# Optimization experiments

Hardware: AMD Instinct MI355X
Metric: run time of the kernel (lower is better)

The kernel has to match this reference:

```python
import jax, jax.numpy as jnp
import numpy as np

B, D, L = 16, 64, 2048
NUM_TOKENS = 8192


def setup_inputs() -> dict:
    key = jax.random.key(0)
    k1, k2 = jax.random.split(key)
    z_e = jax.random.normal(k1, (B, D, L), dtype=jnp.float32)
    codebook = jax.random.normal(k2, (NUM_TOKENS, D), dtype=jnp.float32)
    return {"z_e": z_e, "codebook": codebook}


def reference(z_e, codebook):
    # z_e: [B, D, L] -> per-position vectors [B, L, D]
    x = jnp.transpose(z_e, (0, 2, 1))          # [B, L, D]
    xf = x.reshape(-1, x.shape[-1])            # [N, D], N = B*L
    x2 = jnp.sum(xf * xf, axis=-1, keepdims=True)            # [N, 1]
    c2 = jnp.sum(codebook * codebook, axis=-1)               # [K]
    d2 = x2 - 2.0 * (xf @ codebook.T) + c2[None, :]          # [N, K]
    idx = jnp.argmin(d2, axis=-1)                            # [N]
    zq = codebook[idx]                                        # [N, D] gather
    zq = zq.reshape(x.shape)                                  # [B, L, D]
    # straight-through with codebook stop-gradient (code_sg=True)
    zq_st = x + jax.lax.stop_gradient(zq - x)                 # [B, L, D]
    v_q = jnp.transpose(zq_st, (0, 2, 1))                     # [B, D, L]
    indices = idx.reshape(z_e.shape[0], -1)                   # [B, L]
    return v_q, indices
```

## Files before the change

kernel.cpp:

```cpp
#include <hip/hip_runtime.h>
#include <hip/hip_bf16.h>
#include <cstdint>

#define BB 16
#define DD 64
#define LL 2048
#define NQ (BB*LL)
#define KK 8192
#define VQ_SIZE (BB*DD*LL)
#define CHUNK 256
#define NCH (KK/CHUNK)
#define QSL 256
#define QPS (NQ/QSL)
#define MARGIN 0.75f

typedef __attribute__((ext_vector_type(8))) short short8;
typedef __attribute__((ext_vector_type(4))) float f32x4;
typedef unsigned long long u64;


static __device__ inline short f2bf(float f) {
    __hip_bfloat16 h = __float2bfloat16(f);
    return __builtin_bit_cast(short, h);
}

#define FMIN_DPP(v, ctrl)                                                     \
    do {                                                                      \
        int _vi = __float_as_int(v);                                          \
        int _sh = __builtin_amdgcn_update_dpp(_vi, _vi, (ctrl), 0xf, 0xf, false); \
        (v) = fminf((v), __int_as_float(_sh));                                \
    } while (0)

#define FMAX_DPP(v, ctrl)                                                     \
    do {                                                                      \
        int _vi = __float_as_int(v);                                          \
        int _sh = __builtin_amdgcn_update_dpp(_vi, _vi, (ctrl), 0xf, 0xf, false); \
        (v) = fmaxf((v), __int_as_float(_sh));                                \
    } while (0)

__global__ __launch_bounds__(256) void prep_x(const float* __restrict__ ze,
                                              short* __restrict__ xb) {
    __shared__ float t[64][65];
    const int b = blockIdx.x;
    const int l0 = blockIdx.y * 64;
    const int tid = threadIdx.x;
    #pragma unroll
    for (int it = 0; it < 4; ++it) {
        int id = it * 256 + tid;
        int d = id >> 4;
        int lw = (id & 15) * 4;
        const float4 v = *(const float4*)(ze + ((size_t)b * DD + d) * LL + l0 + lw);
        t[d][lw + 0] = v.x; t[d][lw + 1] = v.y; t[d][lw + 2] = v.z; t[d][lw + 3] = v.w;
    }
    __syncthreads();
    #pragma unroll
    for (int it = 0; it < 2; ++it) {
        int id = it * 256 + tid;
        int lr = id >> 3;
        int u = id & 7;
        short8 o;
        #pragma unroll
        for (int e = 0; e < 8; ++e) o[e] = f2bf(t[u * 8 + e][lr]);
        *(short8*)(xb + (size_t)(b * LL + l0 + lr) * DD + u * 8) = o;
    }
}

__global__ __launch_bounds__(256) void prep_xf(const float* __restrict__ ze,
                                               float* __restrict__ xf) {
    __shared__ float t[64][65];
    const int b = blockIdx.x;
    const int l0 = blockIdx.y * 64;
    const int tid = threadIdx.x;
    #pragma unroll
    for (int it = 0; it < 4; ++it) {
        int id = it * 256 + tid;
        int d = id >> 4;
        int lw = (id & 15) * 4;
        const float4 v = *(const float4*)(ze + ((size_t)b * DD + d) * LL + l0 + lw);
        t[d][lw + 0] = v.x; t[d][lw + 1] = v.y; t[d][lw + 2] = v.z; t[d][lw + 3] = v.w;
    }
    __syncthreads();
    #pragma unroll
    for (int it = 0; it < 4; ++it) {
        int id = it * 256 + tid;
        int row = id >> 4;
        int u = id & 15;
        float4 o = make_float4(t[4 * u + 0][row], t[4 * u + 1][row],
                               t[4 * u + 2][row], t[4 * u + 3][row]);
        *(float4*)(xf + (size_t)(b * LL + l0 + row) * DD + u * 4) = o;
    }
}

__global__ __launch_bounds__(256) void prep_nh2(const float* __restrict__ cbf,
                                                float* __restrict__ nh2) {
    int k = blockIdx.x * 256 + threadIdx.x;
    const float4* c4 = (const float4*)(cbf + (size_t)k * DD);
    float s = 0.f;
    #pragma unroll
    for (int i = 0; i < DD / 4; ++i) {
        float4 v = c4[i];
        s += v.x * v.x + v.y * v.y + v.z * v.z + v.w * v.w;
    }
    nh2[k] = -0.5f * s;
}

__global__ __launch_bounds__(256) void vq_screen(const float* __restrict__ cbf,
                                                 const float* __restrict__ nh2,
                                                 const short* __restrict__ xb,
                                                 float* __restrict__ cmaxT) {
    __shared__ short cbt[CHUNK * 64];
    __shared__ float sh2[CHUNK];
    const int tid = threadIdx.x;
    const int lane = tid & 63;
    const int wid = tid >> 6;
    const int kbase = blockIdx.y * CHUNK;
    const int qbase = blockIdx.x * 512 + wid * 128;
    const int r16 = lane & 15, g = lane >> 4;

    #pragma unroll
    for (int it = 0; it < 8; ++it) {
        int id = it * 256 + tid;
        int row = id >> 3;
        int u = id & 7;
        const float4 lo = *(const float4*)(cbf + (size_t)(kbase + row) * 64 + u * 8);
        const float4 hi = *(const float4*)(cbf + (size_t)(kbase + row) * 64 + u * 8 + 4);
        short8 o;
        o[0] = f2bf(lo.x); o[1] = f2bf(lo.y); o[2] = f2bf(lo.z); o[3] = f2bf(lo.w);
        o[4] = f2bf(hi.x); o[5] = f2bf(hi.y); o[6] = f2bf(hi.z); o[7] = f2bf(hi.w);
        *(short8*)(&cbt[row * 64 + ((u ^ (row & 7)) * 8)]) = o;
    }
    sh2[tid] = nh2[kbase + tid];
    __syncthreads();

    short8 a[8][2];
    #pragma unroll
    for (int t = 0; t < 8; ++t)
        #pragma unroll
        for (int ks = 0; ks < 2; ++ks)
            a[t][ks] = *(const short8*)(xb + (size_t)(qbase + t * 16 + r16) * 64 + ks * 32 + g * 8);

    float rm[8][4];
    #pragma unroll
    for (int t = 0; t < 8; ++t)
        #pragma unroll
        for (int j = 0; j < 4; ++j) rm[t][j] = -3.4e38f;

    for (int cs = 0; cs < CHUNK / 16; ++cs) {
        const int rowb = cs * 16 + r16;
        const float nh = sh2[rowb];
        const f32x4 ci = {nh, nh, nh, nh};
        const short8 b0 = *(const short8*)(&cbt[rowb * 64 + ((g ^ (rowb & 7)) * 8)]);
        const short8 b1 = *(const short8*)(&cbt[rowb * 64 + (((g + 4) ^ (rowb & 7)) * 8)]);
        #pragma unroll
        for (int t = 0; t < 8; ++t) {
            f32x4 acc = __builtin_amdgcn_mfma_f32_16x16x32_bf16(a[t][0], b0, ci, 0, 0, 0);
            acc = __builtin_amdgcn_mfma_f32_16x16x32_bf16(a[t][1], b1, acc, 0, 0, 0);
            rm[t][0] = fmaxf(rm[t][0], acc[0]);
            rm[t][1] = fmaxf(rm[t][1], acc[1]);
            rm[t][2] = fmaxf(rm[t][2], acc[2]);
            rm[t][3] = fmaxf(rm[t][3], acc[3]);
        }
    }

    #pragma unroll
    for (int t = 0; t < 8; ++t)
        #pragma unroll
        for (int j = 0; j < 4; ++j) {
            FMAX_DPP(rm[t][j], 0x111);
            FMAX_DPP(rm[t][j], 0x112);
            FMAX_DPP(rm[t][j], 0x114);
            FMAX_DPP(rm[t][j], 0x118);
        }

    if (r16 == 15) {
        #pragma unroll
        for (int t = 0; t < 8; ++t)
            #pragma unroll
            for (int j = 0; j < 4; ++j)
                cmaxT[(size_t)blockIdx.y * NQ + (qbase + t * 16 + g * 4 + j)] = rm[t][j];
    }
}

__global__ __launch_bounds__(256) void vq_cand(const float* __restrict__ cmaxT,
                                               u64* __restrict__ qmask,
                                               u64* __restrict__ keys) {
    const int tid = threadIdx.x;
    const int lane = tid & 63;
    const int q = blockIdx.x * 256 + tid;
    const int qword = q >> 6;
    float v[NCH];
    float m = -3.4e38f;
    #pragma unroll
    for (int j = 0; j < NCH; ++j) {
        v[j] = cmaxT[(size_t)j * NQ + q];
        m = fmaxf(m, v[j]);
    }
    keys[q] = ~0ULL;
    const float thr = m - MARGIN;
    #pragma unroll
    for (int j = 0; j < NCH; ++j) {
        u64 mm = __ballot(v[j] >= thr);
        if (lane == 0) qmask[(size_t)j * (NQ / 64) + qword] = mm;
    }
}

__global__ __launch_bounds__(256, 2) void vq_exact(const float* __restrict__ xf,
                                                   const float* __restrict__ cbf,
                                                   const float* __restrict__ nh2,
                                                   const u64* __restrict__ qmask,
                                                   u64* __restrict__ keys) {
    const int ch = blockIdx.x;
    const int slice = blockIdx.y;
    const int lane = threadIdx.x & 63;
    const int wid = threadIdx.x >> 6;
    const int kb = ch * CHUNK + wid * 64;
    const int k = kb + lane;

    const u64* wm = qmask + (size_t)ch * (NQ / 64) + slice * (QPS / 64);
    u64 words[QPS / 64];
    u64 any = 0;
    #pragma unroll
    for (int w = 0; w < QPS / 64; ++w) {
        u64 x = wm[w];
        uint32_t lo = __builtin_amdgcn_readfirstlane((uint32_t)x);
        uint32_t hi = __builtin_amdgcn_readfirstlane((uint32_t)(x >> 32));
        words[w] = ((u64)hi << 32) | lo;
        any |= words[w];
    }
    if (!any) return;

    f32x4 cdv[16];
    const f32x4* cb4 = (const f32x4*)(cbf + (size_t)k * DD);
    #pragma unroll
    for (int i = 0; i < 16; ++i) cdv[i] = cb4[i];
    const float nh2k = nh2[k];

    #pragma unroll 1
    for (int w = 0; w < QPS / 64; ++w) {
        u64 sw = words[w];
        while (sw) {
            const int bit = __ffsll((long long)sw) - 1;
            sw &= sw - 1;
            const int q = slice * QPS + w * 64 + bit;
            const f32x4* xr4 = (const f32x4*)(xf + (size_t)q * DD);
            f32x4 xv[16];
            #pragma unroll
            for (int i = 0; i < 16; ++i) xv[i] = xr4[i];

            float a0 = 0.f, a1 = 0.f, a2 = 0.f, a3 = 0.f;
            #pragma unroll
            for (int i = 0; i < 16; ++i) {
                a0 = fmaf(xv[i].x, cdv[i].x, a0);
                a1 = fmaf(xv[i].y, cdv[i].y, a1);
                a2 = fmaf(xv[i].z, cdv[i].z, a2);
                a3 = fmaf(xv[i].w, cdv[i].w, a3);
            }
            float val = -(((a0 + a1) + (a2 + a3)) + nh2k);

            float mn = val;
            FMIN_DPP(mn, 0x111);
            FMIN_DPP(mn, 0x112);
            FMIN_DPP(mn, 0x114);
            FMIN_DPP(mn, 0x118);
            FMIN_DPP(mn, 0x142);
            FMIN_DPP(mn, 0x143);
            const float mnall = __uint_as_float(
                __builtin_amdgcn_readlane(__float_as_uint(mn), 63));

            u64 mk = __ballot(val == mnall);
            int srcl = __ffsll((long long)mk) - 1;
            uint32_t uu = __float_as_uint(mnall);
            uint32_t ub = ((int)uu < 0) ? ~uu : (uu | 0x80000000u);
            u64 key = ((u64)ub << 32) | (unsigned)(kb + srcl);
            if (lane == 0) atomicMin(&keys[q], key);
        }
    }
}

__global__ __launch_bounds__(256) void vq_gather(const float* __restrict__ cb,
                                                 const u64* __restrict__ keys,
                                                 float* __restrict__ vq,
                                                 float* __restrict__ oidx) {
    int t = blockIdx.x * 256 + threadIdx.x;
    int l = t & (LL - 1);
    int bd = t >> 11;
    int d = bd & 63;
    int b = bd >> 6;
    int idx = (int)(unsigned)(keys[b * LL + l] & 0x1FFFu);
    vq[t] = cb[idx * DD + d];
    if (d == 0) oidx[b * LL + l] = (float)idx;
}

extern "C" void kernel_launch(void* const* d_in, const int* in_sizes, int n_in,
                              void* d_out, int out_size, void* d_ws, size_t ws_size,
                              hipStream_t stream) {
    const float* ze = (const float*)d_in[0];
    const float* cb = (const float*)d_in[1];
    float* out = (float*)d_out;

    short* xb = (short*)d_out;
    float* cmaxT = (float*)((char*)d_out + (size_t)NQ * DD * 2);
    float* xf = (float*)d_out;
    u64* qmask = (u64*)(out + VQ_SIZE);
    float* nh2 = (float*)d_ws;
    u64* keys = (u64*)((char*)d_ws + (size_t)KK * 4);
    float* oidx = out + VQ_SIZE;

    dim3 gx(BB, LL / 64);
    prep_x<<<gx, 256, 0, stream>>>(ze, xb);
    prep_nh2<<<KK / 256, 256, 0, stream>>>(cb, nh2);

    dim3 gs(NQ / 512, NCH);
    vq_screen<<<gs, 256, 0, stream>>>(cb, nh2, xb, cmaxT);

    vq_cand<<<NQ / 256, 256, 0, stream>>>(cmaxT, qmask, keys);

    prep_xf<<<gx, 256, 0, stream>>>(ze, xf);

    dim3 ge(NCH, QSL);
    vq_exact<<<ge, 256, 0, stream>>>(xf, cb, nh2, qmask, keys);

    vq_gather<<<VQ_SIZE / 256, 256, 0, stream>>>(cb, keys, out, oidx);
}
```

Baseline: 153.8 us.

## Screen codebook at 128-entry granularity with fp16 maxima and per-query masks

Result: slower. 158.7 us (+3.1%).

```diff
diff --git a/kernel.cpp b/kernel.cpp
--- a/kernel.cpp
+++ b/kernel.cpp
@@ -1,5 +1,6 @@
 #include <hip/hip_runtime.h>
 #include <hip/hip_bf16.h>
+#include <hip/hip_fp16.h>
 #include <cstdint>
 
 #define BB 16
@@ -10,9 +11,10 @@
 #define VQ_SIZE (BB*DD*LL)
 #define CHUNK 256
 #define NCH (KK/CHUNK)
+#define NG 64
 #define QSL 256
 #define QPS (NQ/QSL)
-#define MARGIN 0.75f
+#define MARGIN 0.80f
 
 typedef __attribute__((ext_vector_type(8))) short short8;
 typedef __attribute__((ext_vector_type(4))) float f32x4;
@@ -107,14 +109,14 @@
 __global__ __launch_bounds__(256) void vq_screen(const float* __restrict__ cbf,
                                                  const float* __restrict__ nh2,
                                                  const short* __restrict__ xb,
-                                                 float* __restrict__ cmaxT) {
+                                                 __half* __restrict__ cmaxG) {
     __shared__ short cbt[CHUNK * 64];
     __shared__ float sh2[CHUNK];
     const int tid = threadIdx.x;
     const int lane = tid & 63;
     const int wid = tid >> 6;
     const int kbase = blockIdx.y * CHUNK;
-    const int qbase = blockIdx.x * 512 + wid * 128;
+    const int qbase = blockIdx.x * 256 + wid * 64;
     const int r16 = lane & 15, g = lane >> 4;
 
     #pragma unroll
@@ -132,19 +134,22 @@
     sh2[tid] = nh2[kbase + tid];
     __syncthreads();
 
-    short8 a[8][2];
-    #pragma unroll
-    for (int t = 0; t < 8; ++t)
+    short8 a[4][2];
+    #pragma unroll
+    for (int t = 0; t < 4; ++t)
         #pragma unroll
         for (int ks = 0; ks < 2; ++ks)
             a[t][ks] = *(const short8*)(xb + (size_t)(qbase + t * 16 + r16) * 64 + ks * 32 + g * 8);
 
-    float rm[8][4];
-    #pragma unroll
-    for (int t = 0; t < 8; ++t)
-        #pragma unroll
-        for (int j = 0; j < 4; ++j) rm[t][j] = -3.4e38f;
-
+    float rm[2][4][4];
+    #pragma unroll
+    for (int h = 0; h < 2; ++h)
+        #pragma unroll
+        for (int t = 0; t < 4; ++t)
+            #pragma unroll
+            for (int j = 0; j < 4; ++j) rm[h][t][j] = -3.4e38f;
+
+    #pragma unroll
     for (int cs = 0; cs < CHUNK / 16; ++cs) {
         const int rowb = cs * 16 + r16;
         const float nh = sh2[rowb];
@@ -152,62 +157,76 @@
         const short8 b0 = *(const short8*)(&cbt[rowb * 64 + ((g ^ (rowb & 7)) * 8)]);
         const short8 b1 = *(const short8*)(&cbt[rowb * 64 + (((g + 4) ^ (rowb & 7)) * 8)]);
         #pragma unroll
-        for (int t = 0; t < 8; ++t) {
+        for (int t = 0; t < 4; ++t) {
             f32x4 acc = __builtin_amdgcn_mfma_f32_16x16x32_bf16(a[t][0], b0, ci, 0, 0, 0);
             acc = __builtin_amdgcn_mfma_f32_16x16x32_bf16(a[t][1], b1, acc, 0, 0, 0);
-            rm[t][0] = fmaxf(rm[t][0], acc[0]);
-            rm[t][1] = fmaxf(rm[t][1], acc[1]);
-            rm[t][2] = fmaxf(rm[t][2], acc[2]);
-            rm[t][3] = fmaxf(rm[t][3], acc[3]);
+            rm[cs >> 3][t][0] = fmaxf(rm[cs >> 3][t][0], acc[0]);
+            rm[cs >> 3][t][1] = fmaxf(rm[cs >> 3][t][1], acc[1]);
+            rm[cs >> 3][t][2] = fmaxf(rm[cs >> 3][t][2], acc[2]);
+            rm[cs >> 3][t][3] = fmaxf(rm[cs >> 3][t][3], acc[3]);
         }
     }
 
     #pragma unroll
-    for (int t = 0; t < 8; ++t)
-        #pragma unroll
-        for (int j = 0; j < 4; ++j) {
-            FMAX_DPP(rm[t][j], 0x111);
-            FMAX_DPP(rm[t][j], 0x112);
-            FMAX_DPP(rm[t][j], 0x114);
-            FMAX_DPP(rm[t][j], 0x118);
-        }
+    for (int h = 0; h < 2; ++h)
+        #pragma unroll
+        for (int t = 0; t < 4; ++t)
+            #pragma unroll
+            for (int j = 0; j < 4; ++j) {
+                FMAX_DPP(rm[h][t][j], 0x111);
+                FMAX_DPP(rm[h][t][j], 0x112);
+                FMAX_DPP(rm[h][t][j], 0x114);
+                FMAX_DPP(rm[h][t][j], 0x118);
+            }
 
     if (r16 == 15) {
         #pragma unroll
-        for (int t = 0; t < 8; ++t)
-            #pragma unroll
-            for (int j = 0; j < 4; ++j)
-                cmaxT[(size_t)blockIdx.y * NQ + (qbase + t * 16 + g * 4 + j)] = rm[t][j];
-    }
-}
-
-__global__ __launch_bounds__(256) void vq_cand(const float* __restrict__ cmaxT,
-                                               u64* __restrict__ qmask,
+        for (int h = 0; h < 2; ++h)
+            #pragma unroll
+            for (int t = 0; t < 4; ++t)
+                #pragma unroll
+                for (int j = 0; j < 4; ++j)
+                    cmaxG[(size_t)(blockIdx.y * 2 + h) * NQ + (qbase + t * 16 + g * 4 + j)] =
+                        __float2half_rd(rm[h][t][j]);
+    }
+}
+
+template <bool FINE>
+__global__ __launch_bounds__(256) void vq_cand(const __half* __restrict__ cmaxG,
+                                               u64* __restrict__ mask64,
+                                               uint32_t* __restrict__ mask32,
                                                u64* __restrict__ keys) {
-    const int tid = threadIdx.x;
-    const int lane = tid & 63;
-    const int q = blockIdx.x * 256 + tid;
-    const int qword = q >> 6;
-    float v[NCH];
+    const int q = blockIdx.x * 256 + threadIdx.x;
     float m = -3.4e38f;
     #pragma unroll
-    for (int j = 0; j < NCH; ++j) {
-        v[j] = cmaxT[(size_t)j * NQ + q];
-        m = fmaxf(m, v[j]);
-    }
+    for (int j = 0; j < NG; ++j)
+        m = fmaxf(m, __half2float(cmaxG[(size_t)j * NQ + q]));
     keys[q] = ~0ULL;
     const float thr = m - MARGIN;
-    #pragma unroll
-    for (int j = 0; j < NCH; ++j) {
-        u64 mm = __ballot(v[j] >= thr);
-        if (lane == 0) qmask[(size_t)j * (NQ / 64) + qword] = mm;
-    }
-}
-
+    if (FINE) {
+        u64 mm = 0;
+        #pragma unroll
+        for (int j = 0; j < NG; ++j)
+            if (__half2float(cmaxG[(size_t)j * NQ + q]) >= thr) mm |= (1ULL << j);
+        mask64[q] = mm;
+    } else {
+        uint32_t mm = 0;
+        #pragma unroll
+        for (int j = 0; j < NCH; ++j) {
+            bool a0 = __half2float(cmaxG[(size_t)(2 * j) * NQ + q]) >= thr;
+            bool a1 = __half2float(cmaxG[(size_t)(2 * j + 1) * NQ + q]) >= thr;
+            if (a0 || a1) mm |= (1u << j);
+        }
+        mask32[q] = mm;
+    }
+}
+
+template <bool FINE>
 __global__ __launch_bounds__(256, 2) void vq_exact(const float* __restrict__ xf,
                                                    const float* __restrict__ cbf,
                                                    const float* __restrict__ nh2,
-                                                   const u64* __restrict__ qmask,
+                                                   const u64* __restrict__ mask64,
+                                                   const uint32_t* __restrict__ mask32,
                                                    u64* __restrict__ keys) {
     const int ch = blockIdx.x;
     const int slice = blockIdx.y;
@@ -215,19 +234,31 @@
     const int wid = threadIdx.x >> 6;
     const int kb = ch * CHUNK + wid * 64;
     const int k = kb + lane;
-
-    const u64* wm = qmask + (size_t)ch * (NQ / 64) + slice * (QPS / 64);
-    u64 words[QPS / 64];
-    u64 any = 0;
-    #pragma unroll
-    for (int w = 0; w < QPS / 64; ++w) {
-        u64 x = wm[w];
-        uint32_t lo = __builtin_amdgcn_readfirstlane((uint32_t)x);
-        uint32_t hi = __builtin_amdgcn_readfirstlane((uint32_t)(x >> 32));
-        words[w] = ((u64)hi << 32) | lo;
-        any |= words[w];
-    }
-    if (!any) return;
+    const int qs = slice * QPS;
+
+    u64 b0, b1;
+    if (FINE) {
+        const int grp = ch * 2 + (wid >> 1);
+        u64 m0 = mask64[qs + lane];
+        u64 m1 = mask64[qs + 64 + lane];
+        b0 = __ballot(((m0 >> grp) & 1ULL) != 0);
+        b1 = __ballot(((m1 >> grp) & 1ULL) != 0);
+    } else {
+        uint32_t m0 = mask32[qs + lane];
+        uint32_t m1 = mask32[qs + 64 + lane];
+        b0 = __ballot(((m0 >> ch) & 1u) != 0);
+        b1 = __ballot(((m1 >> ch) & 1u) != 0);
+    }
+    u64 words[2];
+    {
+        uint32_t lo = __builtin_amdgcn_readfirstlane((uint32_t)b0);
+        uint32_t hi = __builtin_amdgcn_readfirstlane((uint32_t)(b0 >> 32));
+        words[0] = ((u64)hi << 32) | lo;
+        lo = __builtin_amdgcn_readfirstlane((uint32_t)b1);
+        hi = __builtin_amdgcn_readfirstlane((uint32_t)(b1 >> 32));
+        words[1] = ((u64)hi << 32) | lo;
+    }
+    if (!(words[0] | words[1])) return;
 
     f32x4 cdv[16];
     const f32x4* cb4 = (const f32x4*)(cbf + (size_t)k * DD);
@@ -236,12 +267,12 @@
     const float nh2k = nh2[k];
 
     #pragma unroll 1
-    for (int w = 0; w < QPS / 64; ++w) {
+    for (int w = 0; w < 2; ++w) {
         u64 sw = words[w];
         while (sw) {
             const int bit = __ffsll((long long)sw) - 1;
             sw &= sw - 1;
-            const int q = slice * QPS + w * 64 + bit;
+            const int q = qs + w * 64 + bit;
             const f32x4* xr4 = (const f32x4*)(xf + (size_t)q * DD);
             f32x4 xv[16];
             #pragma unroll
@@ -299,26 +330,31 @@
     float* out = (float*)d_out;
 
     short* xb = (short*)d_out;
-    float* cmaxT = (float*)((char*)d_out + (size_t)NQ * DD * 2);
+    __half* cmaxG = (__half*)((char*)d_out + (size_t)NQ * DD * 2);
     float* xf = (float*)d_out;
-    u64* qmask = (u64*)(out + VQ_SIZE);
     float* nh2 = (float*)d_ws;
     u64* keys = (u64*)((char*)d_ws + (size_t)KK * 4);
+    u64* mask64 = (u64*)((char*)d_ws + (size_t)288 * 1024);
+    uint32_t* mask32 = (uint32_t*)(out + VQ_SIZE);
     float* oidx = out + VQ_SIZE;
+
+    const bool fine = ws_size >= (size_t)(544 * 1024);
 
     dim3 gx(BB, LL / 64);
     prep_x<<<gx, 256, 0, stream>>>(ze, xb);
     prep_nh2<<<KK / 256, 256, 0, stream>>>(cb, nh2);
 
-    dim3 gs(NQ / 512, NCH);
-    vq_screen<<<gs, 256, 0, stream>>>(cb, nh2, xb, cmaxT);
-
-    vq_cand<<<NQ / 256, 256, 0, stream>>>(cmaxT, qmask, keys);
+    dim3 gs(NQ / 256, NCH);
+    vq_screen<<<gs, 256, 0, stream>>>(cb, nh2, xb, cmaxG);
+
+    if (fine) vq_cand<true><<<NQ / 256, 256, 0, stream>>>(cmaxG, mask64, mask32, keys);
+    else      vq_cand<false><<<NQ / 256, 256, 0, stream>>>(cmaxG, mask64, mask32, keys);
 
     prep_xf<<<gx, 256, 0, stream>>>(ze, xf);
 
     dim3 ge(NCH, QSL);
-    vq_exact<<<ge, 256, 0, stream>>>(xf, cb, nh2, qmask, keys);
+    if (fine) vq_exact<true><<<ge, 256, 0, stream>>>(xf, cb, nh2, mask64, mask32, keys);
+    else      vq_exact<false><<<ge, 256, 0, stream>>>(xf, cb, nh2, mask64, mask32, keys);
 
     vq_gather<<<VQ_SIZE / 256, 256, 0, stream>>>(cb, keys, out, oidx);
 }
```
